# Kernel optimization log

Measured on AMD Instinct MI355X. Metric: run time of the kernel, lower is better.

## Reference

```python
import jax, jax.numpy as jnp
import numpy as np

DIM = 512
HEADS = 8
DIM_HEAD = 64          # dim // 8
M = 256                # num_landmarks = dim // 2
PINV_ITERS = 6
SCALE = DIM_HEAD ** -0.5
KERNEL = 33            # residual_conv_kernel


def setup_inputs() -> dict:
    key = jax.random.key(0)
    ks = jax.random.split(key, 5)
    b, n = 4, 4096  # n divisible by M -> no padding branch
    inner = HEADS * DIM_HEAD
    x = jax.random.normal(ks[0], (b, n, DIM), jnp.float32)
    ln_w = jnp.ones((DIM,), jnp.float32)
    ln_b = jnp.zeros((DIM,), jnp.float32)
    w_qkv = jax.random.normal(ks[1], (DIM, 3 * inner), jnp.float32) / np.sqrt(DIM)
    w_out = jax.random.normal(ks[2], (inner, DIM), jnp.float32) / np.sqrt(inner)
    b_out = jnp.zeros((DIM,), jnp.float32)
    # depthwise Conv2d(heads, heads, (33,1), groups=heads, bias=False): weight [H,1,33,1]
    w_res = jax.random.normal(ks[3], (HEADS, 1, KERNEL, 1), jnp.float32) * 0.05
    return dict(x=x, ln_w=ln_w, ln_b=ln_b, w_qkv=w_qkv, w_out=w_out, b_out=b_out, w_res=w_res)


def moore_penrose_iter_pinv(x, iters=PINV_ITERS):
    # x: (..., m, m) row-stochastic softmax matrix
    abs_x = jnp.abs(x)
    col = abs_x.sum(-1).max()   # global max, matches torch.max(col)
    row = abs_x.sum(-2).max()
    z = jnp.swapaxes(x, -1, -2) / (col * row)
    I = jnp.eye(x.shape[-1], dtype=x.dtype)
    for _ in range(iters):
        xz = x @ z
        z = 0.25 * z @ (13 * I - xz @ (15 * I - xz @ (7 * I - xz)))
    return z


def reference(x, ln_w, ln_b, w_qkv, w_out, b_out, w_res):
    b, n, d = x.shape
    # pre-norm LayerNorm (eps=1e-5, biased variance)
    mu = x.mean(-1, keepdims=True)
    var = ((x - mu) ** 2).mean(-1, keepdims=True)
    h = (x - mu) * jax.lax.rsqrt(var + 1e-5) * ln_w + ln_b

    qkv = h @ w_qkv                           # (b, n, 3*inner)
    q, k, v = jnp.split(qkv, 3, axis=-1)
    to_heads = lambda t: t.reshape(b, n, HEADS, DIM_HEAD).transpose(0, 2, 1, 3)
    q = to_heads(q) * SCALE                   # (b, h, n, d)
    k = to_heads(k)
    v = to_heads(v)

    # landmarks: mean over consecutive chunks of size l = n // M
    l = n // M
    q_l = q.reshape(b, HEADS, M, l, DIM_HEAD).mean(3)  # (b, h, m, d)
    k_l = k.reshape(b, HEADS, M, l, DIM_HEAD).mean(3)

    sim1 = jnp.einsum('bhid,bhjd->bhij', q, k_l)       # (b, h, n, m)
    sim2 = jnp.einsum('bhid,bhjd->bhij', q_l, k_l)     # (b, h, m, m)
    sim3 = jnp.einsum('bhid,bhjd->bhij', q_l, k)       # (b, h, m, n)
    attn1 = jax.nn.softmax(sim1, -1)
    attn2 = jax.nn.softmax(sim2, -1)
    attn3 = jax.nn.softmax(sim3, -1)

    attn2_inv = moore_penrose_iter_pinv(attn2)
    out = (attn1 @ attn2_inv) @ (attn3 @ v)            # (b, h, n, d)

    # residual depthwise conv over sequence dim, per head
    pad = KERNEL // 2
    res = jax.lax.conv_general_dilated(
        v, w_res, window_strides=(1, 1), padding=((pad, pad), (0, 0)),
        dimension_numbers=('NCHW', 'OIHW', 'NCHW'), feature_group_count=HEADS)
    out = out + res

    out = out.transpose(0, 2, 1, 3).reshape(b, n, HEADS * DIM_HEAD)
    out = out @ w_out + b_out                          # to_out (dropout=identity in eval)
    return x + out
```

## Files before the change

kernel.cpp:

```cpp
#include <hip/hip_runtime.h>
#include <hip/hip_bf16.h>
#include <hip/hip_fp16.h>

#define B_ 4
#define H_ 8
#define N_ 4096
#define DH_ 64
#define D_ 512
#define M_ 256
#define BH_ 32
#define NT_ 16384

typedef unsigned short u16;
using sh8 = __attribute__((ext_vector_type(8))) short;
using sh4 = __attribute__((ext_vector_type(4))) short;
using f4  = __attribute__((ext_vector_type(4))) float;

__device__ __forceinline__ float bf2f(u16 u){ return __uint_as_float(((unsigned)u)<<16); }
__device__ __forceinline__ u16 f2bf(float f){
  unsigned u = __float_as_uint(f);
  u += 0x7fffu + ((u>>16)&1u);
  return (u16)(u>>16);
}

__global__ __launch_bounds__(256) void ln_kernel(const float* __restrict__ x,
    const float* __restrict__ w, const float* __restrict__ b, u16* __restrict__ h){
  int row = blockIdx.x;
  const float2* xr = (const float2*)(x + (size_t)row*D_);
  int t = threadIdx.x;
  float2 v = xr[t];
  float s = v.x+v.y, ss = v.x*v.x+v.y*v.y;
  #pragma unroll
  for (int o=32;o;o>>=1){ s += __shfl_xor(s,o); ss += __shfl_xor(ss,o); }
  __shared__ float sb[4], sb2[4];
  if ((t&63)==0){ sb[t>>6]=s; sb2[t>>6]=ss; }
  __syncthreads();
  float ts  = sb[0]+sb[1]+sb[2]+sb[3];
  float tss = sb2[0]+sb2[1]+sb2[2]+sb2[3];
  float mean = ts*(1.f/D_);
  float var  = tss*(1.f/D_) - mean*mean;
  float rstd = rsqrtf(var+1e-5f);
  int c = 2*t;
  float o0 = (v.x-mean)*rstd*w[c]   + b[c];
  float o1 = (v.y-mean)*rstd*w[c+1] + b[c+1];
  u16* hr = h + (size_t)row*D_;
  hr[c] = f2bf(o0); hr[c+1] = f2bf(o1);
}

__global__ void castT2_kernel(const float* __restrict__ wqkv, u16* __restrict__ wqkvT,
    const float* __restrict__ wout, u16* __restrict__ woutT){
  int idx = blockIdx.x*256 + threadIdx.x;
  if (idx < 512*1536){
    int k = idx/1536, n = idx - k*1536;
    wqkvT[(size_t)n*512 + k] = f2bf(wqkv[idx]);
  } else {
    int i2 = idx - 512*1536;
    if (i2 < 512*512){
      int k = i2>>9, n = i2&511;
      woutT[(size_t)n*512 + k] = f2bf(wout[i2]);
    }
  }
}

__global__ __launch_bounds__(256) void gemm_qkv(const u16* __restrict__ A,
    const u16* __restrict__ Bt, u16* __restrict__ q, u16* __restrict__ k, u16* __restrict__ v){
  __shared__ __align__(16) short sm[2*128*72];
  short* As = sm; short* Bs = sm + 128*72;
  int r0 = blockIdx.x*128, c0 = blockIdx.y*128;
  int tid = threadIdx.x, lane = tid&63, w = tid>>6;
  int wr = w>>1, wc = w&1;
  f4 acc[4][4];
  #pragma unroll
  for (int i=0;i<4;i++){
    #pragma unroll
    for (int j=0;j<4;j++) acc[i][j]=0;
  }
  for (int kt=0;kt<8;kt++){
    __syncthreads();
    #pragma unroll
    for (int i=0;i<4;i++){
      int c = i*256+tid, row = c>>3, kg = c&7;
      *(sh8*)&As[row*72+kg*8] = *(const sh8*)(A + (size_t)(r0+row)*512 + kt*64 + kg*8);
      *(sh8*)&Bs[row*72+kg*8] = *(const sh8*)(Bt + (size_t)(c0+row)*512 + kt*64 + kg*8);
    }
    __syncthreads();
    #pragma unroll
    for (int kc=0;kc<2;kc++){
      sh8 a[4], bq[4];
      #pragma unroll
      for (int fr=0;fr<4;fr++) a[fr]  = *(const sh8*)&As[(wr*64+fr*16+(lane&15))*72 + kc*32 + ((lane>>4)<<3)];
      #pragma unroll
      for (int fc=0;fc<4;fc++) bq[fc] = *(const sh8*)&Bs[(wc*64+fc*16+(lane&15))*72 + kc*32 + ((lane>>4)<<3)];
      #pragma unroll
      for (int fr=0;fr<4;fr++){
        #pragma unroll
        for (int fc=0;fc<4;fc++)
          acc[fr][fc] = __builtin_amdgcn_mfma_f32_16x16x32_bf16(a[fr], bq[fc], acc[fr][fc], 0,0,0);
      }
    }
  }
  float* tb = (float*)sm;
  #pragma unroll 1
  for (int pass=0; pass<2; pass++){
    __syncthreads();
    if (wr==pass){
      #pragma unroll
      for (int fr=0;fr<4;fr++){
        #pragma unroll
        for (int fc=0;fc<4;fc++){
          #pragma unroll
          for (int j=0;j<4;j++)
            tb[(fr*16+((lane>>4)<<2)+j)*132 + wc*64+fc*16+(lane&15)] = acc[fr][fc][j];
        }
      }
    }
    __syncthreads();
    #pragma unroll
    for (int i=0;i<4;i++){
      int ch = i*256+tid;
      int lr = ch>>4, cq = (ch&15)*8;
      int r = r0 + pass*64 + lr;
      int c = c0 + cq;
      int which = c>>9, hh = (c>>6)&7, d = c&63;
      int bb = r>>12, n = r&4095;
      float scale = (which==0)? 0.125f : 1.f;
      sh8 ov;
      #pragma unroll
      for (int jj=0;jj<8;jj++) ov[jj] = (short)f2bf(tb[lr*132+cq+jj]*scale);
      u16* dst = which==0 ? q : (which==1 ? k : v);
      *(sh8*)(dst + (((size_t)(bb*8+hh))*4096 + n)*64 + d) = ov;
    }
  }
}

__global__ __launch_bounds__(64) void landmark_kernel(const u16* __restrict__ q,
    const u16* __restrict__ k, u16* __restrict__ ql, u16* __restrict__ kl){
  int bh = blockIdx.x, m = blockIdx.y, d = threadIdx.x;
  const u16* qp = q + (((size_t)bh*4096) + m*16)*64 + d;
  const u16* kp = k + (((size_t)bh*4096) + m*16)*64 + d;
  float sq=0, sk=0;
  #pragma unroll
  for (int j=0;j<16;j++){ sq += bf2f(qp[j*64]); sk += bf2f(kp[j*64]); }
  ql[((size_t)bh*256+m)*64+d] = f2bf(sq*(1.f/16.f));
  kl[((size_t)bh*256+m)*64+d] = f2bf(sk*(1.f/16.f));
}

__global__ __launch_bounds__(256) void attn2_kernel(const u16* __restrict__ ql,
    const u16* __restrict__ kl, u16* __restrict__ Xhi, u16* __restrict__ Xlo){
  int bh = blockIdx.x, rb = blockIdx.y;
  __shared__ short klds[256*72];
  const u16* kg = kl + (size_t)bh*256*64;
  int tid = threadIdx.x;
  #pragma unroll
  for (int i=0;i<8;i++){
    int c = i*256+tid, row = c>>3, kgi = c&7;
    *(sh8*)&klds[row*72+kgi*8] = *(const sh8*)(kg + row*64 + kgi*8);
  }
  __syncthreads();
  int r = rb*16 + (tid>>4), t = tid&15;
  const u16* qr = ql + ((size_t)bh*256 + r)*64;
  float qv[64];
  #pragma unroll
  for (int i=0;i<8;i++){
    sh8 v8 = *(const sh8*)(qr + i*8);
    #pragma unroll
    for (int j=0;j<8;j++) qv[i*8+j] = bf2f((u16)v8[j]);
  }
  float s[16];
  #pragma unroll
  for (int j=0;j<16;j++){
    int col = t + 16*j;
    const short* kr = &klds[col*72];
    float accv=0;
    #pragma unroll
    for (int i8=0;i8<8;i8++){
      sh8 kv = *(const sh8*)(kr + i8*8);
      #pragma unroll
      for (int jj=0;jj<8;jj++) accv += qv[i8*8+jj]*bf2f((u16)kv[jj]);
    }
    s[j]=accv;
  }
  float mx = s[0];
  #pragma unroll
  for (int j=1;j<16;j++) mx = fmaxf(mx, s[j]);
  #pragma unroll
  for (int o=1;o<16;o<<=1) mx = fmaxf(mx, __shfl_xor(mx,o));
  float sum=0;
  #pragma unroll
  for (int j=0;j<16;j++){ s[j] = __expf(s[j]-mx); sum += s[j]; }
  #pragma unroll
  for (int o=1;o<16;o<<=1) sum += __shfl_xor(sum,o);
  float inv = 1.f/sum;
  u16* Xh = Xhi + ((size_t)bh*256 + r)*256;
  u16* Xl = Xlo + ((size_t)bh*256 + r)*256;
  #pragma unroll
  for (int j=0;j<16;j++){
    float val = s[j]*inv;
    u16 hb = f2bf(val);
    Xh[t+16*j] = hb; Xl[t+16*j] = f2bf(val - bf2f(hb));
  }
}

__global__ __launch_bounds__(256) void colrow_kernel(const u16* __restrict__ Xhi,
    const u16* __restrict__ Xlo, float* __restrict__ scal){
  int bh = blockIdx.x, t = threadIdx.x;
  const u16* xh = Xhi + (size_t)bh*65536;
  const u16* xl = Xlo + (size_t)bh*65536;
  float cs=0, rs=0;
  for (int m=0;m<256;m++) cs += bf2f(xh[m*256+t]) + bf2f(xl[m*256+t]);
  for (int c=0;c<256;c++) rs += bf2f(xh[t*256+c]) + bf2f(xl[t*256+c]);
  #pragma unroll
  for (int o=32;o;o>>=1){ cs = fmaxf(cs, __shfl_xor(cs,o)); rs = fmaxf(rs, __shfl_xor(rs,o)); }
  __shared__ float sb[4], sb2[4];
  if ((t&63)==0){ sb[t>>6]=cs; sb2[t>>6]=rs; }
  __syncthreads();
  if (t==0){
    float mc = fmaxf(fmaxf(sb[0],sb[1]),fmaxf(sb[2],sb[3]));
    float mr = fmaxf(fmaxf(sb2[0],sb2[1]),fmaxf(sb2[2],sb2[3]));
    atomicMax((unsigned*)&scal[1], __float_as_uint(mc));
    atomicMax((unsigned*)&scal[0], __float_as_uint(mr));
  }
}

__global__ __launch_bounds__(256) void ztinit_kernel(const u16* __restrict__ Xhi,
    const u16* __restrict__ Xlo, const float* __restrict__ scal,
    u16* __restrict__ Zhi, u16* __restrict__ Zlo, u16* __restrict__ ZThi, u16* __restrict__ ZTlo){
  int bh = blockIdx.x; int xr0 = blockIdx.y*64, xc0 = blockIdx.z*64;
  __shared__ float tb[64*66];
  float inv = 1.f/(scal[0]*scal[1]);
  int tid = threadIdx.x;
  size_t mo = (size_t)bh*65536;
  int row = tid>>2, cof = (tid&3)*16;
  #pragma unroll
  for (int s2=0;s2<2;s2++){
    sh8 hv = *(const sh8*)(Xhi + mo + (size_t)(xr0+row)*256 + xc0+cof+s2*8);
    sh8 lv = *(const sh8*)(Xlo + mo + (size_t)(xr0+row)*256 + xc0+cof+s2*8);
    #pragma unroll
    for (int j=0;j<8;j++) tb[row*66 + cof+s2*8+j] = (bf2f((u16)hv[j])+bf2f((u16)lv[j]))*inv;
  }
  __syncthreads();
  int lc = tid&63;
  #pragma unroll
  for (int i=0;i<16;i++){
    int lr = i*4 + (tid>>6);
    float v1 = tb[lr*66+lc];
    u16 h1 = f2bf(v1);
    ZThi[mo + (size_t)(xr0+lr)*256 + xc0+lc] = h1;
    ZTlo[mo + (size_t)(xr0+lr)*256 + xc0+lc] = f2bf(v1 - bf2f(h1));
    float v2 = tb[lc*66+lr];
    u16 h2 = f2bf(v2);
    Zhi[mo + (size_t)(xc0+lr)*256 + xr0+lc] = h2;
    Zlo[mo + (size_t)(xc0+lr)*256 + xr0+lc] = f2bf(v2 - bf2f(h2));
  }
}

template<int LO>
__device__ __forceinline__ void pinv_body(
    const u16* __restrict__ Ahi, const u16* __restrict__ Alo,
    const u16* __restrict__ Bthi, const u16* __restrict__ Btlo,
    const u16* __restrict__ E1hi, const u16* __restrict__ E1lo,
    const u16* __restrict__ E2hi, const u16* __restrict__ E2lo,
    u16* __restrict__ Chi, u16* __restrict__ Clo,
    u16* __restrict__ CThi, u16* __restrict__ CTlo,
    float k0, float k1, float k2, int bh, int r0, int col0,
    short* smem){
  size_t mo = (size_t)bh*65536;
  int tid=threadIdx.x, lane=tid&63, w=tid>>6, wr=w>>1, wc=w&1;
  int srow = tid>>2, skof = (tid&3)*8;
  const u16* pA  = Ahi  + mo + (size_t)(r0+srow)*256 + skof;
  const u16* pAl = Alo  + mo + (size_t)(r0+srow)*256 + skof;
  const u16* pB  = Bthi + mo + (size_t)(col0+srow)*256 + skof;
  const u16* pBl = Btlo + mo + (size_t)(col0+srow)*256 + skof;
  float e1v[2][2][4], e2v[2][2][4];
  if (E1hi){
    #pragma unroll
    for (int fr=0;fr<2;fr++){
      #pragma unroll
      for (int fc=0;fc<2;fc++){
        #pragma unroll
        for (int j=0;j<4;j++){
          int lr = wr*32+fr*16+((lane>>4)<<2)+j, lc = wc*32+fc*16+(lane&15);
          size_t o = mo+(size_t)(r0+lr)*256+col0+lc;
          e1v[fr][fc][j] = bf2f(E1hi[o]) + (LO ? bf2f(E1lo[o]) : 0.f);
        }
      }
    }
  }
  if (E2hi){
    #pragma unroll
    for (int fr=0;fr<2;fr++){
      #pragma unroll
      for (int fc=0;fc<2;fc++){
        #pragma unroll
        for (int j=0;j<4;j++){
          int lr = wr*32+fr*16+((lane>>4)<<2)+j, lc = wc*32+fc*16+(lane&15);
          size_t o = mo+(size_t)(r0+lr)*256+col0+lc;
          e2v[fr][fc][j] = bf2f(E2hi[o]) + (LO ? bf2f(E2lo[o]) : 0.f);
        }
      }
    }
  }
  sh8 ra  = *(const sh8*)(pA);
  sh8 rb  = *(const sh8*)(pB);
  sh8 ral{}, rbl{};
  if (LO){ ral = *(const sh8*)(pAl); rbl = *(const sh8*)(pBl); }
  f4 acc[2][2];
  #pragma unroll
  for (int i=0;i<2;i++){
    #pragma unroll
    for (int j=0;j<2;j++) acc[i][j]=0;
  }
  for (int kt=0;kt<8;kt++){
    short* Ah = smem + (kt&1)*10240;
    short* Al = Ah + 2560; short* Bh = Ah + 5120; short* Bl = Ah + 7680;
    *(sh8*)&Ah[srow*40+skof] = ra;
    *(sh8*)&Bh[srow*40+skof] = rb;
    if (LO){
      *(sh8*)&Al[srow*40+skof] = ral;
      *(sh8*)&Bl[srow*40+skof] = rbl;
    }
    __syncthreads();
    if (kt<7){
      int o2 = (kt+1)*32;
      ra  = *(const sh8*)(pA+o2);  rb  = *(const sh8*)(pB+o2);
      if (LO){ ral = *(const sh8*)(pAl+o2); rbl = *(const sh8*)(pBl+o2); }
    }
    sh8 ah[2], al[2], bh8[2], bl8[2];
    #pragma unroll
    for (int fr=0;fr<2;fr++){
      int off = (wr*32+fr*16+(lane&15))*40 + ((lane>>4)<<3);
      ah[fr] = *(const sh8*)&Ah[off];
      if (LO) al[fr] = *(const sh8*)&Al[off];
    }
    #pragma unroll
    for (int fc=0;fc<2;fc++){
      int off = (wc*32+fc*16+(lane&15))*40 + ((lane>>4)<<3);
      bh8[fc] = *(const sh8*)&Bh[off];
      if (LO) bl8[fc] = *(const sh8*)&Bl[off];
    }
    #pragma unroll
    for (int fr=0;fr<2;fr++){
      #pragma unroll
      for (int fc=0;fc<2;fc++){
        acc[fr][fc] = __builtin_amdgcn_mfma_f32_16x16x32_bf16(ah[fr], bh8[fc], acc[fr][fc], 0,0,0);
        if (LO){
          acc[fr][fc] = __builtin_amdgcn_mfma_f32_16x16x32_bf16(ah[fr], bl8[fc], acc[fr][fc], 0,0,0);
          acc[fr][fc] = __builtin_amdgcn_mfma_f32_16x16x32_bf16(al[fr], bh8[fc], acc[fr][fc], 0,0,0);
        }
      }
    }
  }
  __syncthreads();
  float* tb = (float*)smem;
  #pragma unroll
  for (int fr=0;fr<2;fr++){
    #pragma unroll
    for (int fc=0;fc<2;fc++){
      #pragma unroll
      for (int j=0;j<4;j++){
        int lr = wr*32+fr*16+((lane>>4)<<2)+j, lc = wc*32+fc*16+(lane&15);
        float val = k0*acc[fr][fc][j];
        if (E1hi) val += k1*e1v[fr][fc][j];
        if (E2hi) val += k2*e2v[fr][fc][j];
        tb[lr*66+lc] = val;
      }
    }
  }
  __syncthreads();
  int lc2 = tid&63;
  #pragma unroll
  for (int i=0;i<16;i++){
    int lr2 = i*4+(tid>>6);
    if (Chi){
      float v1 = tb[lr2*66+lc2];
      u16 hb=f2bf(v1);
      Chi[mo+(size_t)(r0+lr2)*256+col0+lc2]=hb;
      Clo[mo+(size_t)(r0+lr2)*256+col0+lc2]=f2bf(v1-bf2f(hb));
    }
    if (CThi){
      float v2 = tb[lc2*66 + lr2];
      u16 hb2=f2bf(v2);
      CThi[mo+(size_t)(col0+lr2)*256 + r0+lc2]=hb2;
      CTlo[mo+(size_t)(col0+lr2)*256 + r0+lc2]=f2bf(v2-bf2f(hb2));
    }
  }
}

template<int LO>
__global__ __launch_bounds__(256) void pinv_mm(
    const u16* Ahi, const u16* Alo, const u16* Bthi, const u16* Btlo,
    const u16* E1hi, const u16* E1lo, const u16* E2hi, const u16* E2lo,
    u16* Chi, u16* Clo, u16* CThi, u16* CTlo,
    float k0, float k1, float k2){
  __shared__ __align__(16) short smem[2*10240];
  pinv_body<LO>(Ahi,Alo,Bthi,Btlo,E1hi,E1lo,E2hi,E2lo,Chi,Clo,CThi,CTlo,
            k0,k1,k2, blockIdx.z, blockIdx.x*64, blockIdx.y*64, smem);
}

template<int LO>
__global__ __launch_bounds__(256) void pinv_zupd(
    const u16* Zhi, const u16* Zlo, u16* ZnHi, u16* ZnLo,
    const u16* T1hi, const u16* T1lo,
    u16* TnChi, u16* TnClo, u16* TnThi, u16* TnTlo,
    const u16* Bthi, const u16* Btlo,
    u16* ZTh, u16* ZTl){
  __shared__ __align__(16) short smem[2*10240];
  int which = blockIdx.z >> 5, bh = blockIdx.z & 31;
  const u16* Ah = which ? T1hi : Zhi;
  const u16* Al = which ? T1lo : Zlo;
  u16* Ch  = which ? TnChi : ZnHi;
  u16* Cl  = which ? TnClo : ZnLo;
  u16* CTh = which ? TnThi : ZTh;
  u16* CTl = which ? TnTlo : ZTl;
  pinv_body<LO>(Ah,Al,Bthi,Btlo, Ah,Al, (u16*)0,(u16*)0, Ch,Cl,CTh,CTl,
            -0.25f, 3.25f, 0.f, bh, blockIdx.x*64, blockIdx.y*64, smem);
}

__global__ __launch_bounds__(256) void flash_out3(const u16* __restrict__ qlall,
    const u16* __restrict__ kall, const u16* __restrict__ vall,
    float* __restrict__ part, float2* __restrict__ pms){
  int mt = blockIdx.x, ks = blockIdx.y, bh = blockIdx.z;
  const u16* QL = qlall + ((size_t)bh*256 + mt*128)*64;
  const u16* K  = kall + ((size_t)bh*4096 + (size_t)ks*512)*64;
  const u16* V  = vall + ((size_t)bh*4096 + (size_t)ks*512)*64;
  float* O = part + ((size_t)(bh*8+ks)*256 + (size_t)mt*128)*64;
  float2* MS = pms + (size_t)(bh*8+ks)*256 + mt*128;
  __shared__ __align__(16) short kls[64*72];
  __shared__ __align__(16) short vts[64*72];
  __shared__ __align__(16) short Pls[128*72];
  int tid=threadIdx.x, lane=tid&63, w=tid>>6;
  sh8 aq[2][2];
  #pragma unroll
  for (int fr=0;fr<2;fr++){
    #pragma unroll
    for (int kc=0;kc<2;kc++)
      aq[fr][kc] = *(const sh8*)(QL + (size_t)(w*32+fr*16+(lane&15))*64 + kc*32 + ((lane>>4)<<3));
  }
  f4 oacc[2][4];
  #pragma unroll
  for (int fr=0;fr<2;fr++){
    #pragma unroll
    for (int fc=0;fc<4;fc++) oacc[fr][fc]=0;
  }
  float mrun[2][4], srun[2][4];
  #pragma unroll
  for (int fr=0;fr<2;fr++){
    #pragma unroll
    for (int j=0;j<4;j++){ mrun[fr][j]=-1e30f; srun[fr][j]=0.f; }
  }
  for (int kt=0;kt<8;kt++){
    __syncthreads();
    #pragma unroll
    for (int i=0;i<2;i++){
      int c=i*256+tid, row=c>>3, kg=c&7;
      *(sh8*)&kls[row*72+kg*8] = *(const sh8*)(K + (size_t)(kt*64+row)*64 + kg*8);
    }
    #pragma unroll
    for (int i=0;i<16;i++){
      int c=i*256+tid, d=c&63, nl=c>>6;
      vts[d*72+nl] = (short)V[(size_t)(kt*64+nl)*64 + d];
    }
    __syncthreads();
    f4 sacc[2][4];
    #pragma unroll
    for (int fr=0;fr<2;fr++){
      #pragma unroll
      for (int fc=0;fc<4;fc++) sacc[fr][fc]=0;
    }
    #pragma unroll
    for (int kc=0;kc<2;kc++){
      sh8 bk[4];
      #pragma unroll
      for (int fc=0;fc<4;fc++) bk[fc] = *(const sh8*)&kls[(fc*16+(lane&15))*72 + kc*32 + ((lane>>4)<<3)];
      #pragma unroll
      for (int fr=0;fr<2;fr++){
        #pragma unroll
        for (int fc=0;fc<4;fc++)
          sacc[fr][fc] = __builtin_amdgcn_mfma_f32_16x16x32_bf16(aq[fr][kc], bk[fc], sacc[fr][fc], 0,0,0);
      }
    }
    #pragma unroll
    for (int fr=0;fr<2;fr++){
      #pragma unroll
      for (int j=0;j<4;j++){
        float mt_ = fmaxf(fmaxf(sacc[fr][0][j],sacc[fr][1][j]), fmaxf(sacc[fr][2][j],sacc[fr][3][j]));
        #pragma unroll
        for (int o=1;o<16;o<<=1) mt_ = fmaxf(mt_, __shfl_xor(mt_,o));
        float mnew = fmaxf(mrun[fr][j], mt_);
        float scale = __expf(mrun[fr][j]-mnew);
        float e0 = __expf(sacc[fr][0][j]-mnew);
        float e1 = __expf(sacc[fr][1][j]-mnew);
        float e2 = __expf(sacc[fr][2][j]-mnew);
        float e3 = __expf(sacc[fr][3][j]-mnew);
        sacc[fr][0][j]=e0; sacc[fr][1][j]=e1; sacc[fr][2][j]=e2; sacc[fr][3][j]=e3;
        float sum = (e0+e1)+(e2+e3);
        #pragma unroll
        for (int o=1;o<16;o<<=1) sum += __shfl_xor(sum,o);
        srun[fr][j] = srun[fr][j]*scale + sum;
        mrun[fr][j] = mnew;
        #pragma unroll
        for (int fc=0;fc<4;fc++) oacc[fr][fc][j] *= scale;
      }
    }
    #pragma unroll
    for (int fr=0;fr<2;fr++){
      #pragma unroll
      for (int fc=0;fc<4;fc++){
        #pragma unroll
        for (int j=0;j<4;j++)
          Pls[(w*32+fr*16+((lane>>4)<<2)+j)*72 + fc*16+(lane&15)] = (short)f2bf(sacc[fr][fc][j]);
      }
    }
    #pragma unroll
    for (int kc=0;kc<2;kc++){
      sh8 pa[2], bv[4];
      #pragma unroll
      for (int fr=0;fr<2;fr++) pa[fr] = *(const sh8*)&Pls[(w*32+fr*16+(lane&15))*72 + kc*32 + ((lane>>4)<<3)];
      #pragma unroll
      for (int fc=0;fc<4;fc++) bv[fc] = *(const sh8*)&vts[(fc*16+(lane&15))*72 + kc*32 + ((lane>>4)<<3)];
      #pragma unroll
      for (int fr=0;fr<2;fr++){
        #pragma unroll
        for (int fc=0;fc<4;fc++)
          oacc[fr][fc] = __builtin_amdgcn_mfma_f32_16x16x32_bf16(pa[fr], bv[fc], oacc[fr][fc], 0,0,0);
      }
    }
  }
  #pragma unroll
  for (int fr=0;fr<2;fr++){
    #pragma unroll
    for (int fc=0;fc<4;fc++){
      #pragma unroll
      for (int j=0;j<4;j++)
        O[(size_t)(w*32+fr*16+((lane>>4)<<2)+j)*64 + fc*16+(lane&15)] = oacc[fr][fc][j];
    }
  }
  if ((lane&15)==0){
    #pragma unroll
    for (int fr=0;fr<2;fr++){
      #pragma unroll
      for (int j=0;j<4;j++)
        MS[w*32+fr*16+((lane>>4)<<2)+j] = make_float2(mrun[fr][j], srun[fr][j]);
    }
  }
}

__global__ __launch_bounds__(256) void reduce_o3(const float* __restrict__ part,
    const float2* __restrict__ pms, float* __restrict__ o3){
  int idx = blockIdx.x*256+threadIdx.x;
  int d = idx&63, row = (idx>>6)&255, bh = idx>>14;
  float2 ms[8];
  float M = -1e30f;
  #pragma unroll
  for (int ks=0;ks<8;ks++){
    ms[ks] = pms[(size_t)(bh*8+ks)*256 + row];
    M = fmaxf(M, ms[ks].x);
  }
  float S=0.f, acc=0.f;
  #pragma unroll
  for (int ks=0;ks<8;ks++){
    float e = __expf(ms[ks].x - M);
    S += e*ms[ks].y;
    acc += e*part[((size_t)(bh*8+ks)*256 + row)*64 + d];
  }
  o3[idx] = acc/S;
}

__global__ __launch_bounds__(256) void wt_kernel(const u16* __restrict__ Zhi,
    const u16* __restrict__ Zlo, const float* __restrict__ o3, u16* __restrict__ Wt){
  int bh = blockIdx.x; int m = blockIdx.y*4 + (threadIdx.x>>6); int d = threadIdx.x&63;
  const u16* zh = Zhi + ((size_t)bh*256 + m)*256;
  const u16* zl = Zlo + ((size_t)bh*256 + m)*256;
  const float* op = o3 + (size_t)bh*256*64 + d;
  float accv = 0;
  for (int kk=0;kk<256;kk++) accv += (bf2f(zh[kk])+bf2f(zl[kk]))*op[kk*64];
  Wt[((size_t)bh*64 + d)*256 + m] = f2bf(accv);
}

__global__ __launch_bounds__(256) void fused_out1(const u16* __restrict__ q,
    const u16* __restrict__ klall, const u16* __restrict__ Wtall, u16* __restrict__ Oall){
  int rb = blockIdx.x, bh = blockIdx.y;
  __shared__ __align__(16) short sm[18432];
  short* Bs = sm; short* P = sm;
  int tid=threadIdx.x, lane=tid&63, w=tid>>6;
  const u16* qb  = q + ((size_t)bh*4096 + (size_t)rb*64)*64;
  const u16* klb = klall + (size_t)bh*256*64;
  const u16* Wt  = Wtall + (size_t)bh*64*256;
  #pragma unroll
  for (int i=0;i<8;i++){
    int c = i*256+tid, row = c>>3, kg = c&7;
    *(sh8*)&Bs[row*72+kg*8] = *(const sh8*)(klb + row*64 + kg*8);
  }
  const u16* qrow = qb + (size_t)(w*16+(lane&15))*64 + ((lane>>4)<<3);
  sh8 a0 = *(const sh8*)(qrow);
  sh8 a1 = *(const sh8*)(qrow + 32);
  __syncthreads();
  f4 acc[16];
  #pragma unroll
  for (int fc=0;fc<16;fc++){
    sh8 b0 = *(const sh8*)&Bs[(fc*16+(lane&15))*72 + ((lane>>4)<<3)];
    sh8 b1 = *(const sh8*)&Bs[(fc*16+(lane&15))*72 + 32 + ((lane>>4)<<3)];
    acc[fc]=0;
    acc[fc] = __builtin_amdgcn_mfma_f32_16x16x32_bf16(a0, b0, acc[fc], 0,0,0);
    acc[fc] = __builtin_amdgcn_mfma_f32_16x16x32_bf16(a1, b1, acc[fc], 0,0,0);
  }
  float inv_[4];
  #pragma unroll
  for (int j=0;j<4;j++){
    float m0 = fmaxf(fmaxf(acc[0][j],acc[1][j]), fmaxf(acc[2][j],acc[3][j]));
    float m1 = fmaxf(fmaxf(acc[4][j],acc[5][j]), fmaxf(acc[6][j],acc[7][j]));
    float m2 = fmaxf(fmaxf(acc[8][j],acc[9][j]), fmaxf(acc[10][j],acc[11][j]));
    float m3 = fmaxf(fmaxf(acc[12][j],acc[13][j]), fmaxf(acc[14][j],acc[15][j]));
    float mx = fmaxf(fmaxf(m0,m1), fmaxf(m2,m3));
    #pragma unroll
    for (int o=1;o<16;o<<=1) mx = fmaxf(mx, __shfl_xor(mx,o));
    float e[16];
    #pragma unroll
    for (int fc=0;fc<16;fc++){ e[fc]=__expf(acc[fc][j]-mx); acc[fc][j]=e[fc]; }
    float s = (((e[0]+e[1])+(e[2]+e[3])) + ((e[4]+e[5])+(e[6]+e[7])))
            + (((e[8]+e[9])+(e[10]+e[11])) + ((e[12]+e[13])+(e[14]+e[15])));
    #pragma unroll
    for (int o=1;o<16;o<<=1) s += __shfl_xor(s,o);
    inv_[j] = 1.f/s;
  }
  __syncthreads();
  #pragma unroll
  for (int fc=0;fc<16;fc++){
    #pragma unroll
    for (int j=0;j<4;j++){
      int row = w*16 + ((lane>>4)<<2) + j, col = fc*16 + (lane&15);
      P[row*268 + col] = (short)f2bf(acc[fc][j]*inv_[j]);
    }
  }
  __syncthreads();
  f4 acc2[4];
  #pragma unroll
  for (int fc2=0;fc2<4;fc2++) acc2[fc2]=0;
  sh8 bqA[4], bqB[4];
  #pragma unroll
  for (int fc2=0;fc2<4;fc2++){
    int d = fc2*16 + (lane&15);
    bqA[fc2] = *(const sh8*)(Wt + (size_t)d*256 + ((lane>>4))*8);
  }
  #pragma unroll
  for (int kp=0;kp<4;kp++){
    int kc0 = kp*2, kc1 = kp*2+1;
    #pragma unroll
    for (int fc2=0;fc2<4;fc2++){
      int d = fc2*16 + (lane&15);
      bqB[fc2] = *(const sh8*)(Wt + (size_t)d*256 + (kc1*4+(lane>>4))*8);
    }
    sh8 a = *(const sh8*)&P[(w*16+(lane&15))*268 + kc0*32 + ((lane>>4)<<3)];
    #pragma unroll
    for (int fc2=0;fc2<4;fc2++)
      acc2[fc2] = __builtin_amdgcn_mfma_f32_16x16x32_bf16(a, bqA[fc2], acc2[fc2], 0,0,0);
    if (kp<3){
      #pragma unroll
      for (int fc2=0;fc2<4;fc2++){
        int d = fc2*16 + (lane&15);
        bqA[fc2] = *(const sh8*)(Wt + (size_t)d*256 + ((kc1+1)*4+(lane>>4))*8);
      }
    }
    sh8 a2 = *(const sh8*)&P[(w*16+(lane&15))*268 + kc1*32 + ((lane>>4)<<3)];
    #pragma unroll
    for (int fc2=0;fc2<4;fc2++)
      acc2[fc2] = __builtin_amdgcn_mfma_f32_16x16x32_bf16(a2, bqB[fc2], acc2[fc2], 0,0,0);
  }
  __syncthreads();
  u16* otb = (u16*)sm;
  #pragma unroll
  for (int fc2=0;fc2<4;fc2++){
    #pragma unroll
    for (int j=0;j<4;j++)
      otb[(w*16+((lane>>4)<<2)+j)*72 + fc2*16+(lane&15)] = f2bf(acc2[fc2][j]);
  }
  __syncthreads();
  u16* O = Oall + ((size_t)bh*4096 + (size_t)rb*64)*64;
  #pragma unroll
  for (int i=0;i<2;i++){
    int ch = i*256+tid; int lr = ch>>3, cq = (ch&7)*8;
    sh8 ov = *(sh8*)&otb[lr*72+cq];
    *(sh8*)(O + (size_t)lr*64 + cq) = ov;
  }
}

__global__ __launch_bounds__(256) void combine_kernel(const u16* __restrict__ out1,
    const u16* __restrict__ v, const float* __restrict__ wres, u16* __restrict__ oc){
  int bh = blockIdx.x; int hh = bh&7, bb = bh>>3;
  int n0 = blockIdx.y*64;
  int tid = threadIdx.x, d = tid&63, sub = tid>>6;
  int nbase = n0 + sub*16;
  const u16* vb = v + ((size_t)bh*4096)*64 + d;
  float w_[33];
  #pragma unroll
  for (int j=0;j<33;j++) w_[j] = wres[hh*33+j];
  float vv[48];
  #pragma unroll
  for (int i=0;i<48;i++){
    int nn = nbase + i - 16;
    vv[i] = (nn>=0 && nn<4096) ? bf2f(vb[(size_t)nn*64]) : 0.f;
  }
  #pragma unroll
  for (int r=0;r<16;r++){
    int n = nbase + r;
    float acc = bf2f(out1[(((size_t)bh*4096)+n)*64 + d]);
    #pragma unroll
    for (int j=0;j<33;j++) acc += w_[j]*vv[r+j];
    oc[((size_t)(bb*4096+n))*512 + hh*64 + d] = f2bf(acc);
  }
}

__global__ __launch_bounds__(256) void gemm_final(const u16* __restrict__ A,
    const u16* __restrict__ Bt, const float* __restrict__ x, const float* __restrict__ bo,
    float* __restrict__ out){
  __shared__ short As[128*72], Bs[128*72];
  int r0 = blockIdx.x*128, c0 = blockIdx.y*128;
  int tid = threadIdx.x, lane = tid&63, w = tid>>6;
  int wr = w>>1, wc = w&1;
  f4 acc[4][4];
  #pragma unroll
  for (int i=0;i<4;i++){
    #pragma unroll
    for (int j=0;j<4;j++) acc[i][j]=0;
  }
  for (int kt=0;kt<8;kt++){
    __syncthreads();
    #pragma unroll
    for (int i=0;i<4;i++){
      int c = i*256+tid, row = c>>3, kg = c&7;
      *(sh8*)&As[row*72+kg*8] = *(const sh8*)(A  + (size_t)(r0+row)*512 + kt*64 + kg*8);
      *(sh8*)&Bs[row*72+kg*8] = *(const sh8*)(Bt + (size_t)(c0+row)*512 + kt*64 + kg*8);
    }
    __syncthreads();
    #pragma unroll
    for (int kc=0;kc<2;kc++){
      sh8 a[4], bq[4];
      #pragma unroll
      for (int fr=0;fr<4;fr++) a[fr]  = *(const sh8*)&As[(wr*64+fr*16+(lane&15))*72 + kc*32 + ((lane>>4)<<3)];
      #pragma unroll
      for (int fc=0;fc<4;fc++) bq[fc] = *(const sh8*)&Bs[(wc*64+fc*16+(lane&15))*72 + kc*32 + ((lane>>4)<<3)];
      #pragma unroll
      for (int fr=0;fr<4;fr++){
        #pragma unroll
        for (int fc=0;fc<4;fc++)
          acc[fr][fc] = __builtin_amdgcn_mfma_f32_16x16x32_bf16(a[fr], bq[fc], acc[fr][fc], 0,0,0);
      }
    }
  }
  #pragma unroll
  for (int fr=0;fr<4;fr++){
    #pragma unroll
    for (int fc=0;fc<4;fc++){
      #pragma unroll
      for (int j=0;j<4;j++){
        int r = r0 + wr*64 + fr*16 + ((lane>>4)<<2) + j;
        int c = c0 + wc*64 + fc*16 + (lane&15);
        out[(size_t)r*512+c] = x[(size_t)r*512+c] + acc[fr][fc][j] + bo[c];
      }
    }
  }
}

extern "C" void kernel_launch(void* const* d_in, const int* in_sizes, int n_in,
                              void* d_out, int out_size, void* d_ws, size_t ws_size,
                              hipStream_t stream){
  const float* x    = (const float*)d_in[0];
  const float* lnw  = (const float*)d_in[1];
  const float* lnb  = (const float*)d_in[2];
  const float* wqkv = (const float*)d_in[3];
  const float* wout = (const float*)d_in[4];
  const float* bout = (const float*)d_in[5];
  const float* wres = (const float*)d_in[6];
  float* out = (float*)d_out;

  char* ws = (char*)d_ws;
  size_t off = 0;
  auto alloc = [&](size_t bytes)->void*{ void* p = ws + off; off += (bytes + 255) & ~(size_t)255; return p; };
  u16* h      = (u16*)alloc((size_t)NT_*512*2);
  u16* wqkvT  = (u16*)alloc((size_t)1536*512*2);
  u16* woutT  = (u16*)alloc((size_t)512*512*2);
  u16* k      = (u16*)alloc((size_t)BH_*4096*64*2);
  u16* v      = (u16*)alloc((size_t)BH_*4096*64*2);
  u16* q      = (u16*)alloc((size_t)BH_*4096*64*2);
  float* part = (float*)alloc((size_t)BH_*8*256*64*4);
  float2* pms = (float2*)alloc((size_t)BH_*8*256*8);
  u16* ql     = (u16*)alloc((size_t)BH_*256*64*2);
  u16* kl     = (u16*)alloc((size_t)BH_*256*64*2);
  u16* ZaChi  = (u16*)alloc((size_t)BH_*65536*2);
  u16* ZaClo  = (u16*)alloc((size_t)BH_*65536*2);
  u16* ZbChi  = (u16*)alloc((size_t)BH_*65536*2);
  u16* ZbClo  = (u16*)alloc((size_t)BH_*65536*2);
  u16* scratch = (u16*)alloc((size_t)BH_*65536*2*16);
  float* o3   = (float*)alloc((size_t)BH_*256*64*4);
  u16* Wt     = (u16*)alloc((size_t)BH_*64*256*2);
  float* scal = (float*)alloc(256);
  u16* out1   = scratch;
  u16* oc     = h;

  const size_t C1 = (size_t)BH_*65536;
  u16* base = scratch;
  u16* Xhi   = base + 0*C1;  u16* Xlo   = base + 1*C1;
  u16* T1aCh = base + 2*C1;  u16* T1aCl = base + 3*C1;
  u16* T1aTh = base + 4*C1;  u16* T1aTl = base + 5*C1;
  u16* T1bCh = base + 6*C1;  u16* T1bCl = base + 7*C1;
  u16* T1bTh = base + 8*C1;  u16* T1bTl = base + 9*C1;
  u16* SCh   = base +10*C1;  u16* SCl   = base +11*C1;
  u16* STh   = base +12*C1;  u16* STl   = base +13*C1;
  u16* T3h   = base +14*C1;  u16* T3l   = base +15*C1;
  u16* Z0Th  = SCh;          u16* Z0Tl  = SCl;
  u16* ZTth  = (u16*)part;   u16* ZTtl  = ZTth + C1;

  ln_kernel<<<NT_, 256, 0, stream>>>(x, lnw, lnb, h);
  castT2_kernel<<<(512*1536+512*512+255)/256, 256, 0, stream>>>(wqkv, wqkvT, wout, woutT);
  gemm_qkv<<<dim3(128,12,1), 256, 0, stream>>>(h, wqkvT, q, k, v);
  landmark_kernel<<<dim3(32,256,1), 64, 0, stream>>>(q, k, ql, kl);
  attn2_kernel<<<dim3(32,16,1), 256, 0, stream>>>(ql, kl, Xhi, Xlo);
  hipMemsetAsync(scal, 0, 8, stream);
  colrow_kernel<<<32, 256, 0, stream>>>(Xhi, Xlo, scal);
  ztinit_kernel<<<dim3(32,4,4), 256, 0, stream>>>(Xhi, Xlo, scal, ZaChi, ZaClo, Z0Th, Z0Tl);

  u16* nul = (u16*)0;
  pinv_mm<1><<<dim3(4,4,32),256,0,stream>>>(Xhi,Xlo, Z0Th,Z0Tl, nul,nul,nul,nul,
      T1aCh,T1aCl, T1aTh,T1aTl, 1.f,0.f,0.f);
  u16 *TcCh=T1aCh,*TcCl=T1aCl,*TcTh=T1aTh,*TcTl=T1aTl;
  u16 *TnCh=T1bCh,*TnCl=T1bCl,*TnTh=T1bTh,*TnTl=T1bTl;
  u16 *Zch=ZaChi,*Zcl=ZaClo, *Znh=ZbChi,*Znl=ZbClo;
  for (int it=0; it<6; it++){
    if (it==4){
      pinv_mm<1><<<dim3(4,4,32),256,0,stream>>>(Xhi,Xlo, ZTth,ZTtl, nul,nul,nul,nul,
          TnCh,TnCl, TnTh,TnTl, 1.f,0.f,0.f);
      u16* t;
      t=TcCh;TcCh=TnCh;TnCh=t; t=TcCl;TcCl=TnCl;TnCl=t;
      t=TcTh;TcTh=TnTh;TnTh=t; t=TcTl;TcTl=TnTl;TnTl=t;
    }
    if (it<4){
      pinv_mm<0><<<dim3(4,4,32),256,0,stream>>>(TcCh,TcCl, TcTh,TcTl, nul,nul,nul,nul,
          SCh,SCl, STh,STl, 1.f,0.f,0.f);
      pinv_mm<0><<<dim3(4,4,32),256,0,stream>>>(TcCh,TcCl, STh,STl, TcCh,TcCl, SCh,SCl,
          nul,nul, T3h,T3l, 1.f,15.f,-7.f);
    } else {
      pinv_mm<1><<<dim3(4,4,32),256,0,stream>>>(TcCh,TcCl, TcTh,TcTl, nul,nul,nul,nul,
          SCh,SCl, STh,STl, 1.f,0.f,0.f);
      pinv_mm<1><<<dim3(4,4,32),256,0,stream>>>(TcCh,TcCl, STh,STl, TcCh,TcCl, SCh,SCl,
          nul,nul, T3h,T3l, 1.f,15.f,-7.f);
    }
    if (it<5){
      if (it<4)
        pinv_zupd<0><<<dim3(4,4,64),256,0,stream>>>(Zch,Zcl, Znh,Znl,
            TcCh,TcCl, TnCh,TnCl, TnTh,TnTl, T3h,T3l,
            (it==3)?ZTth:nul, (it==3)?ZTtl:nul);
      else
        pinv_zupd<1><<<dim3(4,4,64),256,0,stream>>>(Zch,Zcl, Znh,Znl,
            TcCh,TcCl, TnCh,TnCl, TnTh,TnTl, T3h,T3l, nul, nul);
      u16* t;
      t=Zch;Zch=Znh;Znh=t; t=Zcl;Zcl=Znl;Znl=t;
      t=TcCh;TcCh=TnCh;TnCh=t; t=TcCl;TcCl=TnCl;TnCl=t;
      t=TcTh;TcTh=TnTh;TnTh=t; t=TcTl;TcTl=TnTl;TnTl=t;
    } else {
      pinv_mm<1><<<dim3(4,4,32),256,0,stream>>>(Zch,Zcl, T3h,T3l, Zch,Zcl, nul,nul,
          Znh,Znl, nul,nul, -0.25f,3.25f,0.f);
    }
  }

  flash_out3<<<dim3(2,8,32),256,0,stream>>>(ql, k, v, part, pms);
  reduce_o3<<<2048, 256, 0, stream>>>(part, pms, o3);
  wt_kernel<<<dim3(32,64,1),256,0,stream>>>(ZaChi, ZaClo, o3, Wt);
  fused_out1<<<dim3(64,32,1),256,0,stream>>>(q, kl, Wt, out1);
  combine_kernel<<<dim3(32,64,1),256,0,stream>>>(out1, v, wres, oc);
  gemm_final<<<dim3(128,4,1),256,0,stream>>>(oc, woutT, x, bout, out);
}
```

Measured before the change: 536.1 us.

## Halve pinv GEMM tile width, vectorize stores, skip unused lo outputs, fuse residual conv

The pinv matmul kernels now use 64x32 output tiles, so twice as many blocks run and the 256x256 batched matmuls fill more of the GPU. The epilogue writes 8-element vectors instead of scalar stores. A template flag skips writing the low-precision halves in the bf16-only iterations, and the unneeded Z transpose outputs are dropped. The residual depthwise conv moves into the out1 kernel, removing a kernel launch and a global round trip of out1, at the cost of more work per block in that kernel.

```diff
diff --git a/kernel.cpp b/kernel.cpp
--- a/kernel.cpp
+++ b/kernel.cpp
@@ -13,7 +13,6 @@
 
 typedef unsigned short u16;
 using sh8 = __attribute__((ext_vector_type(8))) short;
-using sh4 = __attribute__((ext_vector_type(4))) short;
 using f4  = __attribute__((ext_vector_type(4))) float;
 
 __device__ __forceinline__ float bf2f(u16 u){ return __uint_as_float(((unsigned)u)<<16); }
@@ -254,7 +253,7 @@
   }
 }
 
-template<int LO>
+template<int LO, int OUTLO>
 __device__ __forceinline__ void pinv_body(
     const u16* __restrict__ Ahi, const u16* __restrict__ Alo,
     const u16* __restrict__ Bthi, const u16* __restrict__ Btlo,
@@ -265,155 +264,145 @@
     float k0, float k1, float k2, int bh, int r0, int col0,
     short* smem){
   size_t mo = (size_t)bh*65536;
-  int tid=threadIdx.x, lane=tid&63, w=tid>>6, wr=w>>1, wc=w&1;
+  int tid=threadIdx.x, lane=tid&63, w=tid>>6;
   int srow = tid>>2, skof = (tid&3)*8;
-  const u16* pA  = Ahi  + mo + (size_t)(r0+srow)*256 + skof;
-  const u16* pAl = Alo  + mo + (size_t)(r0+srow)*256 + skof;
-  const u16* pB  = Bthi + mo + (size_t)(col0+srow)*256 + skof;
-  const u16* pBl = Btlo + mo + (size_t)(col0+srow)*256 + skof;
-  float e1v[2][2][4], e2v[2][2][4];
+  bool doB = tid < 128;
+  const u16* pA  = Ahi + mo + (size_t)(r0+srow)*256 + skof;
+  const u16* pAl = (LO? Alo : Ahi) + mo + (size_t)(r0+srow)*256 + skof;
+  const u16* pB  = Bthi + mo + (size_t)(col0+(srow&31))*256 + skof;
+  const u16* pBl = (LO? Btlo : Bthi) + mo + (size_t)(col0+(srow&31))*256 + skof;
+  float e1v[2][4], e2v[2][4];
   if (E1hi){
     #pragma unroll
-    for (int fr=0;fr<2;fr++){
-      #pragma unroll
-      for (int fc=0;fc<2;fc++){
-        #pragma unroll
-        for (int j=0;j<4;j++){
-          int lr = wr*32+fr*16+((lane>>4)<<2)+j, lc = wc*32+fc*16+(lane&15);
-          size_t o = mo+(size_t)(r0+lr)*256+col0+lc;
-          e1v[fr][fc][j] = bf2f(E1hi[o]) + (LO ? bf2f(E1lo[o]) : 0.f);
-        }
+    for (int fc=0;fc<2;fc++){
+      #pragma unroll
+      for (int j=0;j<4;j++){
+        int lr = w*16+((lane>>4)<<2)+j, lc = fc*16+(lane&15);
+        size_t o = mo+(size_t)(r0+lr)*256+col0+lc;
+        e1v[fc][j] = bf2f(E1hi[o]) + (LO ? bf2f(E1lo[o]) : 0.f);
       }
     }
   }
   if (E2hi){
     #pragma unroll
-    for (int fr=0;fr<2;fr++){
-      #pragma unroll
-      for (int fc=0;fc<2;fc++){
-        #pragma unroll
-        for (int j=0;j<4;j++){
-          int lr = wr*32+fr*16+((lane>>4)<<2)+j, lc = wc*32+fc*16+(lane&15);
-          size_t o = mo+(size_t)(r0+lr)*256+col0+lc;
-          e2v[fr][fc][j] = bf2f(E2hi[o]) + (LO ? bf2f(E2lo[o]) : 0.f);
-        }
-      }
-    }
-  }
-  sh8 ra  = *(const sh8*)(pA);
-  sh8 rb  = *(const sh8*)(pB);
-  sh8 ral{}, rbl{};
-  if (LO){ ral = *(const sh8*)(pAl); rbl = *(const sh8*)(pBl); }
-  f4 acc[2][2];
-  #pragma unroll
-  for (int i=0;i<2;i++){
-    #pragma unroll
-    for (int j=0;j<2;j++) acc[i][j]=0;
-  }
+    for (int fc=0;fc<2;fc++){
+      #pragma unroll
+      for (int j=0;j<4;j++){
+        int lr = w*16+((lane>>4)<<2)+j, lc = fc*16+(lane&15);
+        size_t o = mo+(size_t)(r0+lr)*256+col0+lc;
+        e2v[fc][j] = bf2f(E2hi[o]) + (LO ? bf2f(E2lo[o]) : 0.f);
+      }
+    }
+  }
+  sh8 ra = *(const sh8*)pA;
+  sh8 ral{}, rbv{}, rbl{};
+  if (LO) ral = *(const sh8*)pAl;
+  if (doB){ rbv = *(const sh8*)pB; if (LO) rbl = *(const sh8*)pBl; }
+  f4 acc[2];
+  acc[0]=0; acc[1]=0;
   for (int kt=0;kt<8;kt++){
-    short* Ah = smem + (kt&1)*10240;
-    short* Al = Ah + 2560; short* Bh = Ah + 5120; short* Bl = Ah + 7680;
+    short* Ah = smem + (kt&1)*7680;
+    short* Al = Ah + 2560; short* Bh = Ah + 5120; short* Bl = Ah + 6400;
     *(sh8*)&Ah[srow*40+skof] = ra;
-    *(sh8*)&Bh[srow*40+skof] = rb;
-    if (LO){
-      *(sh8*)&Al[srow*40+skof] = ral;
-      *(sh8*)&Bl[srow*40+skof] = rbl;
+    if (LO) *(sh8*)&Al[srow*40+skof] = ral;
+    if (doB){
+      *(sh8*)&Bh[(srow&31)*40+skof] = rbv;
+      if (LO) *(sh8*)&Bl[(srow&31)*40+skof] = rbl;
     }
     __syncthreads();
     if (kt<7){
       int o2 = (kt+1)*32;
-      ra  = *(const sh8*)(pA+o2);  rb  = *(const sh8*)(pB+o2);
-      if (LO){ ral = *(const sh8*)(pAl+o2); rbl = *(const sh8*)(pBl+o2); }
-    }
-    sh8 ah[2], al[2], bh8[2], bl8[2];
-    #pragma unroll
-    for (int fr=0;fr<2;fr++){
-      int off = (wr*32+fr*16+(lane&15))*40 + ((lane>>4)<<3);
-      ah[fr] = *(const sh8*)&Ah[off];
-      if (LO) al[fr] = *(const sh8*)&Al[off];
-    }
+      ra = *(const sh8*)(pA+o2);
+      if (LO) ral = *(const sh8*)(pAl+o2);
+      if (doB){ rbv = *(const sh8*)(pB+o2); if (LO) rbl = *(const sh8*)(pBl+o2); }
+    }
+    int aoff = (w*16+(lane&15))*40 + ((lane>>4)<<3);
+    sh8 ah = *(const sh8*)&Ah[aoff];
+    sh8 al8{};
+    if (LO) al8 = *(const sh8*)&Al[aoff];
+    sh8 bh8[2], bl8[2];
     #pragma unroll
     for (int fc=0;fc<2;fc++){
-      int off = (wc*32+fc*16+(lane&15))*40 + ((lane>>4)<<3);
-      bh8[fc] = *(const sh8*)&Bh[off];
-      if (LO) bl8[fc] = *(const sh8*)&Bl[off];
-    }
-    #pragma unroll
-    for (int fr=0;fr<2;fr++){
-      #pragma unroll
-      for (int fc=0;fc<2;fc++){
-        acc[fr][fc] = __builtin_amdgcn_mfma_f32_16x16x32_bf16(ah[fr], bh8[fc], acc[fr][fc], 0,0,0);
-        if (LO){
-          acc[fr][fc] = __builtin_amdgcn_mfma_f32_16x16x32_bf16(ah[fr], bl8[fc], acc[fr][fc], 0,0,0);
-          acc[fr][fc] = __builtin_amdgcn_mfma_f32_16x16x32_bf16(al[fr], bh8[fc], acc[fr][fc], 0,0,0);
-        }
+      int boff = (fc*16+(lane&15))*40 + ((lane>>4)<<3);
+      bh8[fc] = *(const sh8*)&Bh[boff];
+      if (LO) bl8[fc] = *(const sh8*)&Bl[boff];
+    }
+    #pragma unroll
+    for (int fc=0;fc<2;fc++){
+      acc[fc] = __builtin_amdgcn_mfma_f32_16x16x32_bf16(ah, bh8[fc], acc[fc], 0,0,0);
+      if (LO){
+        acc[fc] = __builtin_amdgcn_mfma_f32_16x16x32_bf16(ah, bl8[fc], acc[fc], 0,0,0);
+        acc[fc] = __builtin_amdgcn_mfma_f32_16x16x32_bf16(al8, bh8[fc], acc[fc], 0,0,0);
       }
     }
   }
   __syncthreads();
   float* tb = (float*)smem;
   #pragma unroll
-  for (int fr=0;fr<2;fr++){
-    #pragma unroll
-    for (int fc=0;fc<2;fc++){
-      #pragma unroll
-      for (int j=0;j<4;j++){
-        int lr = wr*32+fr*16+((lane>>4)<<2)+j, lc = wc*32+fc*16+(lane&15);
-        float val = k0*acc[fr][fc][j];
-        if (E1hi) val += k1*e1v[fr][fc][j];
-        if (E2hi) val += k2*e2v[fr][fc][j];
-        tb[lr*66+lc] = val;
-      }
-    }
-  }
-  __syncthreads();
-  int lc2 = tid&63;
-  #pragma unroll
-  for (int i=0;i<16;i++){
-    int lr2 = i*4+(tid>>6);
-    if (Chi){
-      float v1 = tb[lr2*66+lc2];
-      u16 hb=f2bf(v1);
-      Chi[mo+(size_t)(r0+lr2)*256+col0+lc2]=hb;
-      Clo[mo+(size_t)(r0+lr2)*256+col0+lc2]=f2bf(v1-bf2f(hb));
-    }
-    if (CThi){
-      float v2 = tb[lc2*66 + lr2];
-      u16 hb2=f2bf(v2);
-      CThi[mo+(size_t)(col0+lr2)*256 + r0+lc2]=hb2;
-      CTlo[mo+(size_t)(col0+lr2)*256 + r0+lc2]=f2bf(v2-bf2f(hb2));
-    }
-  }
-}
-
-template<int LO>
+  for (int fc=0;fc<2;fc++){
+    #pragma unroll
+    for (int j=0;j<4;j++){
+      int lr = w*16+((lane>>4)<<2)+j, lc = fc*16+(lane&15);
+      float val = k0*acc[fc][j];
+      if (E1hi) val += k1*e1v[fc][j];
+      if (E2hi) val += k2*e2v[fc][j];
+      tb[lr*36+lc] = val;
+    }
+  }
+  __syncthreads();
+  if (Chi){
+    int lr2 = tid>>2, cq=(tid&3)*8;
+    sh8 hi8, lo8;
+    #pragma unroll
+    for (int jj=0;jj<8;jj++){
+      float v1 = tb[lr2*36+cq+jj];
+      u16 hb = f2bf(v1);
+      hi8[jj] = (short)hb; lo8[jj] = (short)f2bf(v1-bf2f(hb));
+    }
+    *(sh8*)(Chi + mo + (size_t)(r0+lr2)*256 + col0+cq) = hi8;
+    if (OUTLO) *(sh8*)(Clo + mo + (size_t)(r0+lr2)*256 + col0+cq) = lo8;
+  }
+  if (CThi){
+    int lrT = tid>>3, cqT=(tid&7)*8;
+    sh8 hi8, lo8;
+    #pragma unroll
+    for (int jj=0;jj<8;jj++){
+      float v2 = tb[(cqT+jj)*36 + lrT];
+      u16 hb = f2bf(v2);
+      hi8[jj] = (short)hb; lo8[jj] = (short)f2bf(v2-bf2f(hb));
+    }
+    *(sh8*)(CThi + mo + (size_t)(col0+lrT)*256 + r0+cqT) = hi8;
+    if (OUTLO) *(sh8*)(CTlo + mo + (size_t)(col0+lrT)*256 + r0+cqT) = lo8;
+  }
+}
+
+template<int LO, int OUTLO>
 __global__ __launch_bounds__(256) void pinv_mm(
     const u16* Ahi, const u16* Alo, const u16* Bthi, const u16* Btlo,
     const u16* E1hi, const u16* E1lo, const u16* E2hi, const u16* E2lo,
     u16* Chi, u16* Clo, u16* CThi, u16* CTlo,
     float k0, float k1, float k2){
-  __shared__ __align__(16) short smem[2*10240];
-  pinv_body<LO>(Ahi,Alo,Bthi,Btlo,E1hi,E1lo,E2hi,E2lo,Chi,Clo,CThi,CTlo,
-            k0,k1,k2, blockIdx.z, blockIdx.x*64, blockIdx.y*64, smem);
-}
-
-template<int LO>
+  __shared__ __align__(16) short smem[2*7680];
+  pinv_body<LO,OUTLO>(Ahi,Alo,Bthi,Btlo,E1hi,E1lo,E2hi,E2lo,Chi,Clo,CThi,CTlo,
+            k0,k1,k2, blockIdx.z, blockIdx.x*64, blockIdx.y*32, smem);
+}
+
+template<int LO, int OUTLO>
 __global__ __launch_bounds__(256) void pinv_zupd(
     const u16* Zhi, const u16* Zlo, u16* ZnHi, u16* ZnLo,
     const u16* T1hi, const u16* T1lo,
     u16* TnChi, u16* TnClo, u16* TnThi, u16* TnTlo,
-    const u16* Bthi, const u16* Btlo,
-    u16* ZTh, u16* ZTl){
-  __shared__ __align__(16) short smem[2*10240];
+    const u16* Bthi, const u16* Btlo){
+  __shared__ __align__(16) short smem[2*7680];
   int which = blockIdx.z >> 5, bh = blockIdx.z & 31;
   const u16* Ah = which ? T1hi : Zhi;
   const u16* Al = which ? T1lo : Zlo;
   u16* Ch  = which ? TnChi : ZnHi;
   u16* Cl  = which ? TnClo : ZnLo;
-  u16* CTh = which ? TnThi : ZTh;
-  u16* CTl = which ? TnTlo : ZTl;
-  pinv_body<LO>(Ah,Al,Bthi,Btlo, Ah,Al, (u16*)0,(u16*)0, Ch,Cl,CTh,CTl,
-            -0.25f, 3.25f, 0.f, bh, blockIdx.x*64, blockIdx.y*64, smem);
+  u16* CTh = which ? TnThi : (u16*)0;
+  u16* CTl = which ? TnTlo : (u16*)0;
+  pinv_body<LO,OUTLO>(Ah,Al,Bthi,Btlo, Ah,Al, (u16*)0,(u16*)0, Ch,Cl,CTh,CTl,
+            -0.25f, 3.25f, 0.f, bh, blockIdx.x*64, blockIdx.y*32, smem);
 }
 
 __global__ __launch_bounds__(256) void flash_out3(const u16* __restrict__ qlall,
@@ -577,9 +566,11 @@
   Wt[((size_t)bh*64 + d)*256 + m] = f2bf(accv);
 }
 
-__global__ __launch_bounds__(256) void fused_out1(const u16* __restrict__ q,
-    const u16* __restrict__ klall, const u16* __restrict__ Wtall, u16* __restrict__ Oall){
+__global__ __launch_bounds__(256) void fused_out1c(const u16* __restrict__ q,
+    const u16* __restrict__ klall, const u16* __restrict__ Wtall,
+    const u16* __restrict__ v, const float* __restrict__ wres, u16* __restrict__ oc){
   int rb = blockIdx.x, bh = blockIdx.y;
+  int hh = bh&7, bb = bh>>3;
   __shared__ __align__(16) short sm[18432];
   short* Bs = sm; short* P = sm;
   int tid=threadIdx.x, lane=tid&63, w=tid>>6;
@@ -675,21 +666,8 @@
       otb[(w*16+((lane>>4)<<2)+j)*72 + fc2*16+(lane&15)] = f2bf(acc2[fc2][j]);
   }
   __syncthreads();
-  u16* O = Oall + ((size_t)bh*4096 + (size_t)rb*64)*64;
-  #pragma unroll
-  for (int i=0;i<2;i++){
-    int ch = i*256+tid; int lr = ch>>3, cq = (ch&7)*8;
-    sh8 ov = *(sh8*)&otb[lr*72+cq];
-    *(sh8*)(O + (size_t)lr*64 + cq) = ov;
-  }
-}
-
-__global__ __launch_bounds__(256) void combine_kernel(const u16* __restrict__ out1,
-    const u16* __restrict__ v, const float* __restrict__ wres, u16* __restrict__ oc){
-  int bh = blockIdx.x; int hh = bh&7, bb = bh>>3;
-  int n0 = blockIdx.y*64;
-  int tid = threadIdx.x, d = tid&63, sub = tid>>6;
-  int nbase = n0 + sub*16;
+  int d = tid&63, sub = tid>>6;
+  int nbase = rb*64 + sub*16;
   const u16* vb = v + ((size_t)bh*4096)*64 + d;
   float w_[33];
   #pragma unroll
@@ -702,11 +680,10 @@
   }
   #pragma unroll
   for (int r=0;r<16;r++){
-    int n = nbase + r;
-    float acc = bf2f(out1[(((size_t)bh*4096)+n)*64 + d]);
-    #pragma unroll
-    for (int j=0;j<33;j++) acc += w_[j]*vv[r+j];
-    oc[((size_t)(bb*4096+n))*512 + hh*64 + d] = f2bf(acc);
+    float accv = bf2f(otb[(sub*16+r)*72 + d]);
+    #pragma unroll
+    for (int j=0;j<33;j++) accv += w_[j]*vv[r+j];
+    oc[((size_t)(bb*4096 + nbase + r))*512 + hh*64 + d] = f2bf(accv);
   }
 }
 
@@ -794,7 +771,6 @@
   float* o3   = (float*)alloc((size_t)BH_*256*64*4);
   u16* Wt     = (u16*)alloc((size_t)BH_*64*256*2);
   float* scal = (float*)alloc(256);
-  u16* out1   = scratch;
   u16* oc     = h;
 
   const size_t C1 = (size_t)BH_*65536;
@@ -820,44 +796,51 @@
   ztinit_kernel<<<dim3(32,4,4), 256, 0, stream>>>(Xhi, Xlo, scal, ZaChi, ZaClo, Z0Th, Z0Tl);
 
   u16* nul = (u16*)0;
-  pinv_mm<1><<<dim3(4,4,32),256,0,stream>>>(Xhi,Xlo, Z0Th,Z0Tl, nul,nul,nul,nul,
+  pinv_mm<1,1><<<dim3(4,8,32),256,0,stream>>>(Xhi,Xlo, Z0Th,Z0Tl, nul,nul,nul,nul,
       T1aCh,T1aCl, T1aTh,T1aTl, 1.f,0.f,0.f);
   u16 *TcCh=T1aCh,*TcCl=T1aCl,*TcTh=T1aTh,*TcTl=T1aTl;
   u16 *TnCh=T1bCh,*TnCl=T1bCl,*TnTh=T1bTh,*TnTl=T1bTl;
   u16 *Zch=ZaChi,*Zcl=ZaClo, *Znh=ZbChi,*Znl=ZbClo;
   for (int it=0; it<6; it++){
     if (it==4){
-      pinv_mm<1><<<dim3(4,4,32),256,0,stream>>>(Xhi,Xlo, ZTth,ZTtl, nul,nul,nul,nul,
+      pinv_mm<1,1><<<dim3(4,8,32),256,0,stream>>>(Xhi,Xlo, ZTth,ZTtl, nul,nul,nul,nul,
           TnCh,TnCl, TnTh,TnTl, 1.f,0.f,0.f);
       u16* t;
       t=TcCh;TcCh=TnCh;TnCh=t; t=TcCl;TcCl=TnCl;TnCl=t;
       t=TcTh;TcTh=TnTh;TnTh=t; t=TcTl;TcTl=TnTl;TnTl=t;
     }
     if (it<4){
-      pinv_mm<0><<<dim3(4,4,32),256,0,stream>>>(TcCh,TcCl, TcTh,TcTl, nul,nul,nul,nul,
+      pinv_mm<0,0><<<dim3(4,8,32),256,0,stream>>>(TcCh,TcCl, TcTh,TcTl, nul,nul,nul,nul,
           SCh,SCl, STh,STl, 1.f,0.f,0.f);
-      pinv_mm<0><<<dim3(4,4,32),256,0,stream>>>(TcCh,TcCl, STh,STl, TcCh,TcCl, SCh,SCl,
+      pinv_mm<0,0><<<dim3(4,8,32),256,0,stream>>>(TcCh,TcCl, STh,STl, TcCh,TcCl, SCh,SCl,
           nul,nul, T3h,T3l, 1.f,15.f,-7.f);
     } else {
-      pinv_mm<1><<<dim3(4,4,32),256,0,stream>>>(TcCh,TcCl, TcTh,TcTl, nul,nul,nul,nul,
+      pinv_mm<1,1><<<dim3(4,8,32),256,0,stream>>>(TcCh,TcCl, TcTh,TcTl, nul,nul,nul,nul,
           SCh,SCl, STh,STl, 1.f,0.f,0.f);
-      pinv_mm<1><<<dim3(4,4,32),256,0,stream>>>(TcCh,TcCl, STh,STl, TcCh,TcCl, SCh,SCl,
+      pinv_mm<1,1><<<dim3(4,8,32),256,0,stream>>>(TcCh,TcCl, STh,STl, TcCh,TcCl, SCh,SCl,
           nul,nul, T3h,T3l, 1.f,15.f,-7.f);
     }
-    if (it<5){
-      if (it<4)
-        pinv_zupd<0><<<dim3(4,4,64),256,0,stream>>>(Zch,Zcl, Znh,Znl,
-            TcCh,TcCl, TnCh,TnCl, TnTh,TnTl, T3h,T3l,
-            (it==3)?ZTth:nul, (it==3)?ZTtl:nul);
-      else
-        pinv_zupd<1><<<dim3(4,4,64),256,0,stream>>>(Zch,Zcl, Znh,Znl,
-            TcCh,TcCl, TnCh,TnCl, TnTh,TnTl, T3h,T3l, nul, nul);
+    if (it<3){
+      pinv_zupd<0,0><<<dim3(4,8,64),256,0,stream>>>(Zch,Zcl, Znh,Znl,
+          TcCh,TcCl, TnCh,TnCl, TnTh,TnTl, T3h,T3l);
+      u16* t;
+      t=Zch;Zch=Znh;Znh=t; t=Zcl;Zcl=Znl;Znl=t;
+      t=TcCh;TcCh=TnCh;TnCh=t; t=TcCl;TcCl=TnCl;TnCl=t;
+      t=TcTh;TcTh=TnTh;TnTh=t; t=TcTl;TcTl=TnTl;TnTl=t;
+    } else if (it==3){
+      pinv_mm<0,1><<<dim3(4,8,32),256,0,stream>>>(Zch,Zcl, T3h,T3l, Zch,Zcl, nul,nul,
+          Znh,Znl, ZTth,ZTtl, -0.25f,3.25f,0.f);
+      u16* t;
+      t=Zch;Zch=Znh;Znh=t; t=Zcl;Zcl=Znl;Znl=t;
+    } else if (it==4){
+      pinv_zupd<1,1><<<dim3(4,8,64),256,0,stream>>>(Zch,Zcl, Znh,Znl,
+          TcCh,TcCl, TnCh,TnCl, TnTh,TnTl, T3h,T3l);
       u16* t;
       t=Zch;Zch=Znh;Znh=t; t=Zcl;Zcl=Znl;Znl=t;
       t=TcCh;TcCh=TnCh;TnCh=t; t=TcCl;TcCl=TnCl;TnCl=t;
       t=TcTh;TcTh=TnTh;TnTh=t; t=TcTl;TcTl=TnTl;TnTl=t;
     } else {
-      pinv_mm<1><<<dim3(4,4,32),256,0,stream>>>(Zch,Zcl, T3h,T3l, Zch,Zcl, nul,nul,
+      pinv_mm<1,1><<<dim3(4,8,32),256,0,stream>>>(Zch,Zcl, T3h,T3l, Zch,Zcl, nul,nul,
           Znh,Znl, nul,nul, -0.25f,3.25f,0.f);
     }
   }
@@ -865,7 +848,6 @@
   flash_out3<<<dim3(2,8,32),256,0,stream>>>(ql, k, v, part, pms);
   reduce_o3<<<2048, 256, 0, stream>>>(part, pms, o3);
   wt_kernel<<<dim3(32,64,1),256,0,stream>>>(ZaChi, ZaClo, o3, Wt);
-  fused_out1<<<dim3(64,32,1),256,0,stream>>>(q, kl, Wt, out1);
-  combine_kernel<<<dim3(32,64,1),256,0,stream>>>(out1, v, wres, oc);
+  fused_out1c<<<dim3(64,32,1),256,0,stream>>>(q, kl, Wt, v, wres, oc);
   gemm_final<<<dim3(128,4,1),256,0,stream>>>(oc, woutT, x, bout, out);
 }
```

New measurement: 539.3 us. About the same (+0.6%).
